# Performance work log

Hardware: AMD Instinct MI355X
Metric: run time of the kernel (lower is better)

Reference implementation:

```python
import jax, jax.numpy as jnp
import numpy as np

N_NODES = 100_000
N_EDGES = 1_600_000
HEADS = 3
DIMS = [6, 8, 16, 32]  # in -> conv1 -> conv2 -> conv3 out_feats


def _edge_gat(x, ef, src, dst, W, We, al, ar, ae, b, n_nodes):
    """DGL EdgeGATConv: edge feats modulate attention logits; messages are alpha * W h_src."""
    H, D = al.shape
    ft = (x @ W.T).reshape(n_nodes, H, D)          # [N,H,D] projected node feats
    fe = (ef @ We.T).reshape(-1, H, D)             # [E,H,D] projected edge feats
    el = jnp.sum(ft * al, axis=-1)                 # [N,H]
    er = jnp.sum(ft * ar, axis=-1)                 # [N,H]
    ee = jnp.sum(fe * ae, axis=-1)                 # [E,H]
    e = jax.nn.leaky_relu(el[src] + er[dst] + ee, 0.2)  # [E,H] (DGL default slope 0.2)
    # segment softmax over incoming edges of each dst node
    m = jax.ops.segment_max(e, dst, num_segments=n_nodes)
    m = jnp.where(jnp.isfinite(m), m, 0.0)         # zero-in-degree nodes
    ex = jnp.exp(e - m[dst])
    denom = jax.ops.segment_sum(ex, dst, num_segments=n_nodes)
    a = ex / jnp.maximum(denom[dst], 1e-9)         # [E,H]
    msg = a[:, :, None] * ft[src]                  # [E,H,D]
    out = jax.ops.segment_sum(msg, dst, num_segments=n_nodes)  # [N,H,D]
    return out + b.reshape(1, H, D)


def setup_inputs() -> dict:
    key = jax.random.key(0)
    ks = jax.random.split(key, 32)
    d = {
        "node_feats": jax.random.normal(ks[0], (N_NODES, DIMS[0]), jnp.float32),
        "edge_feats": jax.random.uniform(ks[1], (N_EDGES, 1), jnp.float32),
        "src": jax.random.randint(ks[2], (N_EDGES,), 0, N_NODES, jnp.int32),
        "dst": jax.random.randint(ks[3], (N_EDGES,), 0, N_NODES, jnp.int32),
    }
    ki = 4
    for i in range(3):
        fin, fout = DIMS[i], DIMS[i + 1]
        s = 1.0 / np.sqrt(fin)
        d[f"W{i+1}"] = jax.random.normal(ks[ki], (HEADS * fout, fin), jnp.float32) * s; ki += 1
        d[f"We{i+1}"] = jax.random.normal(ks[ki], (HEADS * fout, 1), jnp.float32); ki += 1
        d[f"al{i+1}"] = jax.random.normal(ks[ki], (HEADS, fout), jnp.float32) * 0.1; ki += 1
        d[f"ar{i+1}"] = jax.random.normal(ks[ki], (HEADS, fout), jnp.float32) * 0.1; ki += 1
        d[f"ae{i+1}"] = jax.random.normal(ks[ki], (HEADS, fout), jnp.float32) * 0.1; ki += 1
        d[f"b{i+1}"] = jnp.zeros((HEADS * fout,), jnp.float32)
    for name, (fo, fi) in [("l1", (16, 32)), ("l2", (4, 16)), ("l3", (1, 4)), ("l4", (1, HEADS))]:
        s = 1.0 / np.sqrt(fi)
        d[name + "w"] = jax.random.uniform(ks[ki], (fo, fi), jnp.float32, -s, s); ki += 1
        d[name + "b"] = jax.random.uniform(ks[ki], (fo,), jnp.float32, -s, s); ki += 1
    return d


def reference(node_feats, edge_feats, src, dst,
              W1, We1, al1, ar1, ae1, b1,
              W2, We2, al2, ar2, ae2, b2,
              W3, We3, al3, ar3, ae3, b3,
              l1w, l1b, l2w, l2b, l3w, l3b, l4w, l4b):
    n = node_feats.shape[0]
    h1 = _edge_gat(node_feats, edge_feats, src, dst, W1, We1, al1, ar1, ae1, b1, n)  # [N,3,8]
    h2 = _edge_gat(h1.mean(axis=1), edge_feats, src, dst, W2, We2, al2, ar2, ae2, b2, n)  # [N,3,16]
    h3 = _edge_gat(h2.mean(axis=1), edge_feats, src, dst, W3, We3, al3, ar3, ae3, b3, n)  # [N,3,32]
    # per-(node,head) MLP head: 32 -> 16 -> 4 -> 1
    x = jax.nn.leaky_relu(h3 @ l1w.T + l1b, 0.01)
    x = jax.nn.leaky_relu(x @ l2w.T + l2b, 0.01)
    x = x @ l3w.T + l3b                            # [N,3,1]
    feats = x.reshape(n, -1) @ l4w.T + l4b         # [N,1] combine heads
    return jnp.max(feats, axis=0)                  # [1]
```

## Files before the change

### kernel.cpp

```cpp
#include <hip/hip_runtime.h>
#include <hip/hip_bf16.h>
#include <hip/hip_fp16.h>

#define HEADS 3

union HU { uint4 u; __half2 h[4]; };

__global__ void prep_ce_kernel(const float* __restrict__ We1, const float* __restrict__ ae1,
                               const float* __restrict__ We2, const float* __restrict__ ae2,
                               const float* __restrict__ We3, const float* __restrict__ ae3,
                               float* __restrict__ ce) {
    int t = threadIdx.x;
    if (t >= 9) return;
    int l = t / 3, h = t % 3;
    const float* We = (l == 0) ? We1 : (l == 1) ? We2 : We3;
    const float* ae = (l == 0) ? ae1 : (l == 1) ? ae2 : ae3;
    int D = (l == 0) ? 8 : (l == 1) ? 16 : 32;
    float s = 0.f;
    for (int d = 0; d < D; d++) s += We[h * D + d] * ae[h * D + d];
    ce[t] = s;
}

__global__ void hist_rank_kernel(const int* __restrict__ dst, int* __restrict__ deg,
                                 int* __restrict__ rank, int E) {
    int tid = blockIdx.x * blockDim.x + threadIdx.x;
    if (tid < E) rank[tid] = atomicAdd(&deg[dst[tid]], 1);
}

#define SCAN_BLK 1024
__global__ void scan1_kernel(const int* __restrict__ deg, int* __restrict__ row_ptr,
                             int* __restrict__ partials, int N) {
    __shared__ int sm[SCAN_BLK];
    int t = threadIdx.x;
    int g = blockIdx.x * SCAN_BLK + t;
    int v = (g < N) ? deg[g] : 0;
    sm[t] = v;
    __syncthreads();
    for (int off = 1; off < SCAN_BLK; off <<= 1) {
        int x = (t >= off) ? sm[t - off] : 0;
        __syncthreads();
        sm[t] += x;
        __syncthreads();
    }
    if (g < N) row_ptr[g] = sm[t] - v;
    if (t == SCAN_BLK - 1) partials[blockIdx.x] = sm[t];
}

__global__ void scan2_kernel(int* __restrict__ partials, int NB) {
    __shared__ int sm[128];
    int t = threadIdx.x;
    int v = (t < NB) ? partials[t] : 0;
    sm[t] = v;
    __syncthreads();
    for (int off = 1; off < 128; off <<= 1) {
        int x = (t >= off) ? sm[t - off] : 0;
        __syncthreads();
        sm[t] += x;
        __syncthreads();
    }
    if (t < NB) partials[t] = sm[t] - v;
    if (t == 127) partials[NB] = sm[127];
}

__global__ void scan3_kernel(int* __restrict__ row_ptr, const int* __restrict__ partials,
                             int N, int NB) {
    int g = blockIdx.x * SCAN_BLK + threadIdx.x;
    if (g < N) row_ptr[g] += partials[blockIdx.x];
    if (blockIdx.x == 0 && threadIdx.x == 0) row_ptr[N] = partials[NB];
}

__global__ void scatter_kernel(const int* __restrict__ src, const int* __restrict__ dst,
                               const float* __restrict__ ef, const int* __restrict__ row_ptr,
                               const int* __restrict__ rank, int2* __restrict__ erec, int E) {
    int tid = blockIdx.x * blockDim.x + threadIdx.x;
    if (tid >= E) return;
    int d = dst[tid];
    int pos = row_ptr[d] + rank[tid];
    union { int2 r; long long ll; } u;
    u.r.x = src[tid];
    u.r.y = __float_as_int(ef[tid]);
    __builtin_nontemporal_store(u.ll, (long long*)&erec[pos]);
}

template <int FIN, int D>
__launch_bounds__(256)
__global__ void node_kernel(const float* __restrict__ xin,
                            const float* __restrict__ W,
                            const float* __restrict__ al,
                            const float* __restrict__ ar,
                            __half* __restrict__ ft,
                            float* __restrict__ el, float* __restrict__ er,
                            int N) {
    int tid = blockIdx.x * blockDim.x + threadIdx.x;
    if (tid >= N * HEADS) return;
    int n = tid / HEADS, h = tid % HEADS;
    float x[FIN];
    #pragma unroll
    for (int k = 0; k < FIN; k++) x[k] = xin[n * FIN + k];
    float fv[D];
    float e_l = 0.f, e_r = 0.f;
    #pragma unroll
    for (int d = 0; d < D; d++) {
        const float* wr = &W[(h * D + d) * FIN];
        float f = 0.f;
        #pragma unroll
        for (int k = 0; k < FIN; k++) f += x[k] * wr[k];
        fv[d] = f;
        e_l += f * al[h * D + d];
        e_r += f * ar[h * D + d];
    }
    uint4* dst16 = (uint4*)(ft + (size_t)tid * D);
    #pragma unroll
    for (int q = 0; q < D / 8; q++) {
        HU u;
        #pragma unroll
        for (int j = 0; j < 4; j++)
            u.h[j] = __floats2half2_rn(fv[q * 8 + 2 * j], fv[q * 8 + 2 * j + 1]);
        dst16[q] = u.u;
    }
    el[tid] = e_l;
    er[tid] = e_r;
}

template <int D, int EPI>
__launch_bounds__(256)
__global__ void agg_kernel(const int* __restrict__ row_ptr, const int2* __restrict__ erec,
                           const __half* __restrict__ ft,
                           const float* __restrict__ el, const float* __restrict__ er,
                           const float* __restrict__ ce,
                           const float* __restrict__ b,
                           float* __restrict__ xmean,
                           __half* __restrict__ h3out,
                           int N) {
    int w = threadIdx.x >> 6;
    int l = threadIdx.x & 63;
    int wl = l / 6;
    int rem = l - wl * 6;
    int s = rem >= 3 ? 1 : 0;
    int h = rem - s * 3;
    int n = (blockIdx.x * 4 + w) * 10 + wl;
    bool active = (wl < 10) && (n < N);

    float m = -3.0e38f, ssum = 0.f;
    float msg[D];
    #pragma unroll
    for (int d = 0; d < D; d++) msg[d] = 0.f;
    int unit = n * HEADS + h;
    float ceh = ce[h];

    if (active) {
        int beg = row_ptr[n], end = row_ptr[n + 1];
        int cnt = end - beg;
        int half = (cnt + 1) >> 1;
        int es = beg + s * half;
        int ee = s ? end : (beg + half);
        float ern = er[unit];

        int e = es;
        for (; e + 3 < ee; e += 4) {
            int2 r0 = erec[e + 0], r1 = erec[e + 1], r2 = erec[e + 2], r3 = erec[e + 3];
            float v0 = el[r0.x * HEADS + h] + ern + __int_as_float(r0.y) * ceh;
            float v1 = el[r1.x * HEADS + h] + ern + __int_as_float(r1.y) * ceh;
            float v2 = el[r2.x * HEADS + h] + ern + __int_as_float(r2.y) * ceh;
            float v3 = el[r3.x * HEADS + h] + ern + __int_as_float(r3.y) * ceh;
            v0 = v0 > 0.f ? v0 : 0.2f * v0;
            v1 = v1 > 0.f ? v1 : 0.2f * v1;
            v2 = v2 > 0.f ? v2 : 0.2f * v2;
            v3 = v3 > 0.f ? v3 : 0.2f * v3;
            float cm = fmaxf(fmaxf(v0, v1), fmaxf(v2, v3));
            if (cm > m) {
                float sc = __expf(m - cm);
                ssum *= sc;
                #pragma unroll
                for (int d = 0; d < D; d++) msg[d] *= sc;
                m = cm;
            }
            float x0 = __expf(v0 - m), x1 = __expf(v1 - m);
            float x2 = __expf(v2 - m), x3 = __expf(v3 - m);
            ssum += (x0 + x1) + (x2 + x3);
            const uint4* f0 = (const uint4*)(ft + ((size_t)r0.x * HEADS + h) * D);
            const uint4* f1 = (const uint4*)(ft + ((size_t)r1.x * HEADS + h) * D);
            const uint4* f2 = (const uint4*)(ft + ((size_t)r2.x * HEADS + h) * D);
            const uint4* f3 = (const uint4*)(ft + ((size_t)r3.x * HEADS + h) * D);
            #pragma unroll
            for (int q = 0; q < D / 8; q++) {
                HU a0, a1, a2, a3;
                a0.u = f0[q]; a1.u = f1[q]; a2.u = f2[q]; a3.u = f3[q];
                #pragma unroll
                for (int j = 0; j < 4; j++) {
                    float2 p0 = __half22float2(a0.h[j]);
                    float2 p1 = __half22float2(a1.h[j]);
                    float2 p2 = __half22float2(a2.h[j]);
                    float2 p3 = __half22float2(a3.h[j]);
                    msg[q * 8 + 2 * j + 0] += x0 * p0.x + x1 * p1.x + x2 * p2.x + x3 * p3.x;
                    msg[q * 8 + 2 * j + 1] += x0 * p0.y + x1 * p1.y + x2 * p2.y + x3 * p3.y;
                }
            }
        }
        for (; e < ee; e++) {
            int2 r = erec[e];
            float v = el[r.x * HEADS + h] + ern + __int_as_float(r.y) * ceh;
            v = v > 0.f ? v : 0.2f * v;
            if (v > m) {
                float sc = __expf(m - v);
                ssum *= sc;
                #pragma unroll
                for (int d = 0; d < D; d++) msg[d] *= sc;
                m = v;
            }
            float x = __expf(v - m);
            ssum += x;
            const uint4* fr = (const uint4*)(ft + ((size_t)r.x * HEADS + h) * D);
            #pragma unroll
            for (int q = 0; q < D / 8; q++) {
                HU a; a.u = fr[q];
                #pragma unroll
                for (int j = 0; j < 4; j++) {
                    float2 p = __half22float2(a.h[j]);
                    msg[q * 8 + 2 * j + 0] += x * p.x;
                    msg[q * 8 + 2 * j + 1] += x * p.y;
                }
            }
        }
    }

    int pl = (s ? (l - 3) : (l + 3)) & 63;
    float om = __shfl(m, pl);
    float osum = __shfl(ssum, pl);
    float M = fmaxf(m, om);
    float sA = __expf(m - M);
    float sB = __expf(om - M);
    float tot = ssum * sA + osum * sB;
    float inv = 1.0f / fmaxf(tot, 1e-9f);
    #pragma unroll
    for (int d = 0; d < D; d++)
        msg[d] = (msg[d] * sA + __shfl(msg[d], pl) * sB) * inv + b[h * D + d];

    if (EPI == 0) {
        int g0 = wl * 6 + s * 3;
        #pragma unroll
        for (int d = 0; d < D; d++)
            msg[d] = (__shfl(msg[d], g0) + __shfl(msg[d], g0 + 1) + __shfl(msg[d], g0 + 2)) * (1.0f / 3.0f);
        if (active && h == 0) {
            int lo = s * (D / 2);
            float* ob = xmean + (size_t)n * D + lo;
            #pragma unroll
            for (int d = 0; d < D / 2; d += 4) {
                float4 v;
                v.x = msg[lo + d + 0]; v.y = msg[lo + d + 1];
                v.z = msg[lo + d + 2]; v.w = msg[lo + d + 3];
                *(float4*)(ob + d) = v;
            }
        }
    } else {
        if (active) {
            int lo = s * (D / 2);
            __half* hb = h3out + ((size_t)n * HEADS + h) * D + lo;
            #pragma unroll
            for (int q = 0; q < D / 16; q++) {
                HU u;
                #pragma unroll
                for (int j = 0; j < 4; j++)
                    u.h[j] = __floats2half2_rn(msg[lo + q * 8 + 2 * j],
                                               msg[lo + q * 8 + 2 * j + 1]);
                *(uint4*)(hb + q * 8) = u.u;
            }
        }
    }
}

__global__ void mlp_max_kernel(const __half* __restrict__ h3,
                               const float* __restrict__ l1w, const float* __restrict__ l1b,
                               const float* __restrict__ l2w, const float* __restrict__ l2b,
                               const float* __restrict__ l3w, const float* __restrict__ l3b,
                               const float* __restrict__ l4w, const float* __restrict__ l4b,
                               unsigned int* __restrict__ maxkey, int N) {
    int tid = blockIdx.x * blockDim.x + threadIdx.x;
    float feat = -3.0e38f;
    if (tid < N) {
        float acc = l4b[0];
        #pragma unroll
        for (int h = 0; h < HEADS; h++) {
            const uint4* vp = (const uint4*)(h3 + ((size_t)tid * HEADS + h) * 32);
            float v[32];
            #pragma unroll
            for (int q = 0; q < 4; q++) {
                HU a; a.u = vp[q];
                #pragma unroll
                for (int j = 0; j < 4; j++) {
                    float2 p = __half22float2(a.h[j]);
                    v[q * 8 + 2 * j + 0] = p.x;
                    v[q * 8 + 2 * j + 1] = p.y;
                }
            }
            float y1[16];
            #pragma unroll
            for (int i = 0; i < 16; i++) {
                float s = l1b[i];
                const float* w = &l1w[i * 32];
                #pragma unroll
                for (int k = 0; k < 32; k++) s += v[k] * w[k];
                y1[i] = s > 0.f ? s : 0.01f * s;
            }
            float y2[4];
            #pragma unroll
            for (int i = 0; i < 4; i++) {
                float s = l2b[i];
                const float* w = &l2w[i * 16];
                #pragma unroll
                for (int k = 0; k < 16; k++) s += y1[k] * w[k];
                y2[i] = s > 0.f ? s : 0.01f * s;
            }
            float y3 = l3b[0];
            #pragma unroll
            for (int k = 0; k < 4; k++) y3 += y2[k] * l3w[k];
            acc += y3 * l4w[h];
        }
        feat = acc;
    }
    #pragma unroll
    for (int off = 32; off > 0; off >>= 1)
        feat = fmaxf(feat, __shfl_down(feat, off));
    if ((threadIdx.x & 63) == 0) {
        unsigned int u = __float_as_uint(feat);
        unsigned int key = (u & 0x80000000u) ? ~u : (u | 0x80000000u);
        atomicMax(maxkey, key);
    }
}

__global__ void finalize_kernel(const unsigned int* __restrict__ maxkey, float* __restrict__ out) {
    unsigned int key = *maxkey;
    unsigned int u = (key & 0x80000000u) ? (key & 0x7FFFFFFFu) : ~key;
    out[0] = __uint_as_float(u);
}

extern "C" void kernel_launch(void* const* d_in, const int* in_sizes, int n_in,
                              void* d_out, int out_size, void* d_ws, size_t ws_size,
                              hipStream_t stream) {
    const float* node_feats = (const float*)d_in[0];
    const float* edge_feats = (const float*)d_in[1];
    const int* src = (const int*)d_in[2];
    const int* dst = (const int*)d_in[3];
    const float* W1  = (const float*)d_in[4];
    const float* We1 = (const float*)d_in[5];
    const float* al1 = (const float*)d_in[6];
    const float* ar1 = (const float*)d_in[7];
    const float* ae1 = (const float*)d_in[8];
    const float* b1  = (const float*)d_in[9];
    const float* W2  = (const float*)d_in[10];
    const float* We2 = (const float*)d_in[11];
    const float* al2 = (const float*)d_in[12];
    const float* ar2 = (const float*)d_in[13];
    const float* ae2 = (const float*)d_in[14];
    const float* b2  = (const float*)d_in[15];
    const float* W3  = (const float*)d_in[16];
    const float* We3 = (const float*)d_in[17];
    const float* al3 = (const float*)d_in[18];
    const float* ar3 = (const float*)d_in[19];
    const float* ae3 = (const float*)d_in[20];
    const float* b3  = (const float*)d_in[21];
    const float* l1w = (const float*)d_in[22];
    const float* l1b = (const float*)d_in[23];
    const float* l2w = (const float*)d_in[24];
    const float* l2b = (const float*)d_in[25];
    const float* l3w = (const float*)d_in[26];
    const float* l3b = (const float*)d_in[27];
    const float* l4w = (const float*)d_in[28];
    const float* l4b = (const float*)d_in[29];

    const int N = in_sizes[0] / 6;
    const int E = in_sizes[2];
    const int NB = (N + SCAN_BLK - 1) / SCAN_BLK;

    char* ws = (char*)d_ws;
    size_t off = 0;
    auto alloc = [&](size_t bytes) -> void* {
        void* p = ws + off;
        off = (off + bytes + 255) & ~(size_t)255;
        return p;
    };
    int* deg            = (int*)alloc((size_t)N * 4);
    unsigned int* mkey  = (unsigned int*)alloc(4);
    size_t zero_bytes   = off;
    int* rank           = (int*)alloc((size_t)E * 4);
    int* row_ptr        = (int*)alloc((size_t)(N + 1) * 4);
    int* partials       = (int*)alloc((size_t)(NB + 1) * 4);
    int2* erec          = (int2*)alloc((size_t)E * 8);
    __half* ft          = (__half*)alloc((size_t)N * 96 * 2);
    __half* h3          = (__half*)alloc((size_t)N * 96 * 2);
    float* xmean        = (float*)alloc((size_t)N * 16 * 4);
    float* el           = (float*)alloc((size_t)N * 3 * 4);
    float* er           = (float*)alloc((size_t)N * 3 * 4);
    float* ce           = (float*)alloc(9 * 4);

    hipMemsetAsync(d_ws, 0, zero_bytes, stream);

    prep_ce_kernel<<<1, 16, 0, stream>>>(We1, ae1, We2, ae2, We3, ae3, ce);
    hist_rank_kernel<<<(E + 255) / 256, 256, 0, stream>>>(dst, deg, rank, E);
    scan1_kernel<<<NB, SCAN_BLK, 0, stream>>>(deg, row_ptr, partials, N);
    scan2_kernel<<<1, 128, 0, stream>>>(partials, NB);
    scan3_kernel<<<NB, SCAN_BLK, 0, stream>>>(row_ptr, partials, N, NB);
    scatter_kernel<<<(E + 255) / 256, 256, 0, stream>>>(src, dst, edge_feats, row_ptr, rank,
                                                        erec, E);

    const int NH = N * HEADS;
    const int gb = (NH + 255) / 256;
    const int gb_agg = (N + 39) / 40;

    node_kernel<6, 8><<<gb, 256, 0, stream>>>(node_feats, W1, al1, ar1, ft, el, er, N);
    agg_kernel<8, 0><<<gb_agg, 256, 0, stream>>>(row_ptr, erec, ft, el, er, ce + 0, b1,
                                                 xmean, nullptr, N);
    node_kernel<8, 16><<<gb, 256, 0, stream>>>(xmean, W2, al2, ar2, ft, el, er, N);
    agg_kernel<16, 0><<<gb_agg, 256, 0, stream>>>(row_ptr, erec, ft, el, er, ce + 3, b2,
                                                  xmean, nullptr, N);
    node_kernel<16, 32><<<gb, 256, 0, stream>>>(xmean, W3, al3, ar3, ft, el, er, N);
    agg_kernel<32, 1><<<gb_agg, 256, 0, stream>>>(row_ptr, erec, ft, el, er, ce + 6, b3,
                                                  nullptr, h3, N);

    mlp_max_kernel<<<(N + 255) / 256, 256, 0, stream>>>(h3, l1w, l1b, l2w, l2b, l3w, l3b,
                                                        l4w, l4b, mkey, N);
    finalize_kernel<<<1, 1, 0, stream>>>(mkey, (float*)d_out);
}
```

Baseline: 463.7 us.

## Sort aggregation nodes by degree and pack layer-1 features with logits

Adds a counting sort of nodes by in-degree (histogram, scan, scatter) so each wavefront in the aggregation kernels processes nodes of similar degree, which reduces lane divergence from imbalanced edge loops. For layer 1, the projected half-precision features and the el logits are packed into one 64-byte record per node, so each gathered source node costs one cache line instead of separate ft and el accesses. This adds three small preprocessing kernels and makes aggregation output writes scattered rather than contiguous.

```diff
diff --git a/kernel.cpp b/kernel.cpp
--- a/kernel.cpp
+++ b/kernel.cpp
@@ -82,12 +82,66 @@
     __builtin_nontemporal_store(u.ll, (long long*)&erec[pos]);
 }
 
-template <int FIN, int D>
+#define OCHUNK 1024
+__global__ void obhist_kernel(const int* __restrict__ deg, int* __restrict__ bh,
+                              int N, int nblk) {
+    __shared__ int hist[64];
+    int t = threadIdx.x;
+    if (t < 64) hist[t] = 0;
+    __syncthreads();
+    int base = blockIdx.x * OCHUNK;
+    for (int i = t; i < OCHUNK; i += 256) {
+        int g = base + i;
+        if (g < N) atomicAdd(&hist[min(deg[g], 63)], 1);
+    }
+    __syncthreads();
+    if (t < 64) bh[t * nblk + blockIdx.x] = hist[t];
+}
+
+__global__ void oscan_kernel(int* __restrict__ bh, int M) {
+    __shared__ int sums[256];
+    int t = threadIdx.x;
+    int C = (M + 255) / 256;
+    int b = t * C, e = min(b + C, M);
+    int s = 0;
+    for (int i = b; i < e; i++) s += bh[i];
+    sums[t] = s;
+    __syncthreads();
+    for (int off = 1; off < 256; off <<= 1) {
+        int x = (t >= off) ? sums[t - off] : 0;
+        __syncthreads();
+        sums[t] += x;
+        __syncthreads();
+    }
+    int run = sums[t] - s;
+    for (int i = b; i < e; i++) { int v = bh[i]; bh[i] = run; run += v; }
+}
+
+__global__ void oscatter_kernel(const int* __restrict__ deg, const int* __restrict__ bh,
+                                int* __restrict__ order, int N, int nblk) {
+    __shared__ int base_[64];
+    __shared__ int cnt_[64];
+    int t = threadIdx.x;
+    if (t < 64) { base_[t] = bh[t * nblk + blockIdx.x]; cnt_[t] = 0; }
+    __syncthreads();
+    int cbase = blockIdx.x * OCHUNK;
+    for (int i = t; i < OCHUNK; i += 256) {
+        int g = cbase + i;
+        if (g < N) {
+            int bin = min(deg[g], 63);
+            int off = atomicAdd(&cnt_[bin], 1);
+            order[base_[bin] + off] = g;
+        }
+    }
+}
+
+template <int FIN, int D, int RECB>
 __launch_bounds__(256)
 __global__ void node_kernel(const float* __restrict__ xin,
                             const float* __restrict__ W,
                             const float* __restrict__ al,
                             const float* __restrict__ ar,
+                            char* __restrict__ rec,
                             __half* __restrict__ ft,
                             float* __restrict__ el, float* __restrict__ er,
                             int N) {
@@ -109,22 +163,38 @@
         e_l += f * al[h * D + d];
         e_r += f * ar[h * D + d];
     }
-    uint4* dst16 = (uint4*)(ft + (size_t)tid * D);
-    #pragma unroll
-    for (int q = 0; q < D / 8; q++) {
-        HU u;
+    if (RECB > 0) {
+        char* rp = rec + (size_t)n * RECB;
+        uint4* dst16 = (uint4*)(rp + h * (D * 2));
         #pragma unroll
-        for (int j = 0; j < 4; j++)
-            u.h[j] = __floats2half2_rn(fv[q * 8 + 2 * j], fv[q * 8 + 2 * j + 1]);
-        dst16[q] = u.u;
-    }
-    el[tid] = e_l;
+        for (int q = 0; q < D / 8; q++) {
+            HU u;
+            #pragma unroll
+            for (int j = 0; j < 4; j++)
+                u.h[j] = __floats2half2_rn(fv[q * 8 + 2 * j], fv[q * 8 + 2 * j + 1]);
+            dst16[q] = u.u;
+        }
+        *(float*)(rp + 3 * D * 2 + h * 4) = e_l;
+    } else {
+        uint4* dst16 = (uint4*)(ft + (size_t)tid * D);
+        #pragma unroll
+        for (int q = 0; q < D / 8; q++) {
+            HU u;
+            #pragma unroll
+            for (int j = 0; j < 4; j++)
+                u.h[j] = __floats2half2_rn(fv[q * 8 + 2 * j], fv[q * 8 + 2 * j + 1]);
+            dst16[q] = u.u;
+        }
+        el[tid] = e_l;
+    }
     er[tid] = e_r;
 }
 
-template <int D, int EPI>
+template <int D, int RECB, int EPI>
 __launch_bounds__(256)
 __global__ void agg_kernel(const int* __restrict__ row_ptr, const int2* __restrict__ erec,
+                           const int* __restrict__ order,
+                           const char* __restrict__ rec,
                            const __half* __restrict__ ft,
                            const float* __restrict__ el, const float* __restrict__ er,
                            const float* __restrict__ ce,
@@ -132,14 +202,16 @@
                            float* __restrict__ xmean,
                            __half* __restrict__ h3out,
                            int N) {
+    const int ELOFF = 3 * D * 2;
     int w = threadIdx.x >> 6;
     int l = threadIdx.x & 63;
     int wl = l / 6;
     int rem = l - wl * 6;
     int s = rem >= 3 ? 1 : 0;
     int h = rem - s * 3;
-    int n = (blockIdx.x * 4 + w) * 10 + wl;
-    bool active = (wl < 10) && (n < N);
+    int slot = (blockIdx.x * 4 + w) * 10 + wl;
+    bool active = (wl < 10) && (slot < N);
+    int n = active ? order[slot] : 0;
 
     float m = -3.0e38f, ssum = 0.f;
     float msg[D];
@@ -159,10 +231,25 @@
         int e = es;
         for (; e + 3 < ee; e += 4) {
             int2 r0 = erec[e + 0], r1 = erec[e + 1], r2 = erec[e + 2], r3 = erec[e + 3];
-            float v0 = el[r0.x * HEADS + h] + ern + __int_as_float(r0.y) * ceh;
-            float v1 = el[r1.x * HEADS + h] + ern + __int_as_float(r1.y) * ceh;
-            float v2 = el[r2.x * HEADS + h] + ern + __int_as_float(r2.y) * ceh;
-            float v3 = el[r3.x * HEADS + h] + ern + __int_as_float(r3.y) * ceh;
+            const char* p0; const char* p1; const char* p2; const char* p3;
+            float v0, v1, v2, v3;
+            if (RECB > 0) {
+                p0 = rec + (size_t)r0.x * RECB; p1 = rec + (size_t)r1.x * RECB;
+                p2 = rec + (size_t)r2.x * RECB; p3 = rec + (size_t)r3.x * RECB;
+                v0 = *(const float*)(p0 + ELOFF + h * 4) + ern + __int_as_float(r0.y) * ceh;
+                v1 = *(const float*)(p1 + ELOFF + h * 4) + ern + __int_as_float(r1.y) * ceh;
+                v2 = *(const float*)(p2 + ELOFF + h * 4) + ern + __int_as_float(r2.y) * ceh;
+                v3 = *(const float*)(p3 + ELOFF + h * 4) + ern + __int_as_float(r3.y) * ceh;
+            } else {
+                p0 = (const char*)(ft + ((size_t)r0.x * HEADS + h) * D);
+                p1 = (const char*)(ft + ((size_t)r1.x * HEADS + h) * D);
+                p2 = (const char*)(ft + ((size_t)r2.x * HEADS + h) * D);
+                p3 = (const char*)(ft + ((size_t)r3.x * HEADS + h) * D);
+                v0 = el[r0.x * HEADS + h] + ern + __int_as_float(r0.y) * ceh;
+                v1 = el[r1.x * HEADS + h] + ern + __int_as_float(r1.y) * ceh;
+                v2 = el[r2.x * HEADS + h] + ern + __int_as_float(r2.y) * ceh;
+                v3 = el[r3.x * HEADS + h] + ern + __int_as_float(r3.y) * ceh;
+            }
             v0 = v0 > 0.f ? v0 : 0.2f * v0;
             v1 = v1 > 0.f ? v1 : 0.2f * v1;
             v2 = v2 > 0.f ? v2 : 0.2f * v2;
@@ -178,28 +265,36 @@
             float x0 = __expf(v0 - m), x1 = __expf(v1 - m);
             float x2 = __expf(v2 - m), x3 = __expf(v3 - m);
             ssum += (x0 + x1) + (x2 + x3);
-            const uint4* f0 = (const uint4*)(ft + ((size_t)r0.x * HEADS + h) * D);
-            const uint4* f1 = (const uint4*)(ft + ((size_t)r1.x * HEADS + h) * D);
-            const uint4* f2 = (const uint4*)(ft + ((size_t)r2.x * HEADS + h) * D);
-            const uint4* f3 = (const uint4*)(ft + ((size_t)r3.x * HEADS + h) * D);
+            const uint4* f0 = (const uint4*)(RECB > 0 ? p0 + h * (D * 2) : p0);
+            const uint4* f1 = (const uint4*)(RECB > 0 ? p1 + h * (D * 2) : p1);
+            const uint4* f2 = (const uint4*)(RECB > 0 ? p2 + h * (D * 2) : p2);
+            const uint4* f3 = (const uint4*)(RECB > 0 ? p3 + h * (D * 2) : p3);
             #pragma unroll
             for (int q = 0; q < D / 8; q++) {
                 HU a0, a1, a2, a3;
                 a0.u = f0[q]; a1.u = f1[q]; a2.u = f2[q]; a3.u = f3[q];
                 #pragma unroll
                 for (int j = 0; j < 4; j++) {
-                    float2 p0 = __half22float2(a0.h[j]);
-                    float2 p1 = __half22float2(a1.h[j]);
-                    float2 p2 = __half22float2(a2.h[j]);
-                    float2 p3 = __half22float2(a3.h[j]);
-                    msg[q * 8 + 2 * j + 0] += x0 * p0.x + x1 * p1.x + x2 * p2.x + x3 * p3.x;
-                    msg[q * 8 + 2 * j + 1] += x0 * p0.y + x1 * p1.y + x2 * p2.y + x3 * p3.y;
+                    float2 p0v = __half22float2(a0.h[j]);
+                    float2 p1v = __half22float2(a1.h[j]);
+                    float2 p2v = __half22float2(a2.h[j]);
+                    float2 p3v = __half22float2(a3.h[j]);
+                    msg[q * 8 + 2 * j + 0] += x0 * p0v.x + x1 * p1v.x + x2 * p2v.x + x3 * p3v.x;
+                    msg[q * 8 + 2 * j + 1] += x0 * p0v.y + x1 * p1v.y + x2 * p2v.y + x3 * p3v.y;
                 }
             }
         }
         for (; e < ee; e++) {
             int2 r = erec[e];
-            float v = el[r.x * HEADS + h] + ern + __int_as_float(r.y) * ceh;
+            const char* pr;
+            float v;
+            if (RECB > 0) {
+                pr = rec + (size_t)r.x * RECB;
+                v = *(const float*)(pr + ELOFF + h * 4) + ern + __int_as_float(r.y) * ceh;
+            } else {
+                pr = (const char*)(ft + ((size_t)r.x * HEADS + h) * D);
+                v = el[r.x * HEADS + h] + ern + __int_as_float(r.y) * ceh;
+            }
             v = v > 0.f ? v : 0.2f * v;
             if (v > m) {
                 float sc = __expf(m - v);
@@ -210,7 +305,7 @@
             }
             float x = __expf(v - m);
             ssum += x;
-            const uint4* fr = (const uint4*)(ft + ((size_t)r.x * HEADS + h) * D);
+            const uint4* fr = (const uint4*)(RECB > 0 ? pr + h * (D * 2) : pr);
             #pragma unroll
             for (int q = 0; q < D / 8; q++) {
                 HU a; a.u = fr[q];
@@ -371,6 +466,7 @@
     const int N = in_sizes[0] / 6;
     const int E = in_sizes[2];
     const int NB = (N + SCAN_BLK - 1) / SCAN_BLK;
+    const int NOB = (N + OCHUNK - 1) / OCHUNK;
 
     char* ws = (char*)d_ws;
     size_t off = 0;
@@ -385,7 +481,10 @@
     int* rank           = (int*)alloc((size_t)E * 4);
     int* row_ptr        = (int*)alloc((size_t)(N + 1) * 4);
     int* partials       = (int*)alloc((size_t)(NB + 1) * 4);
+    int* bh             = (int*)alloc((size_t)(64 * NOB + 1) * 4);
+    int* order          = (int*)alloc((size_t)N * 4);
     int2* erec          = (int2*)alloc((size_t)E * 8);
+    char* rec1          = (char*)alloc((size_t)N * 64);
     __half* ft          = (__half*)alloc((size_t)N * 96 * 2);
     __half* h3          = (__half*)alloc((size_t)N * 96 * 2);
     float* xmean        = (float*)alloc((size_t)N * 16 * 4);
@@ -402,20 +501,24 @@
     scan3_kernel<<<NB, SCAN_BLK, 0, stream>>>(row_ptr, partials, N, NB);
     scatter_kernel<<<(E + 255) / 256, 256, 0, stream>>>(src, dst, edge_feats, row_ptr, rank,
                                                         erec, E);
+    obhist_kernel<<<NOB, 256, 0, stream>>>(deg, bh, N, NOB);
+    oscan_kernel<<<1, 256, 0, stream>>>(bh, 64 * NOB);
+    oscatter_kernel<<<NOB, 256, 0, stream>>>(deg, bh, order, N, NOB);
 
     const int NH = N * HEADS;
     const int gb = (NH + 255) / 256;
     const int gb_agg = (N + 39) / 40;
 
-    node_kernel<6, 8><<<gb, 256, 0, stream>>>(node_feats, W1, al1, ar1, ft, el, er, N);
-    agg_kernel<8, 0><<<gb_agg, 256, 0, stream>>>(row_ptr, erec, ft, el, er, ce + 0, b1,
-                                                 xmean, nullptr, N);
-    node_kernel<8, 16><<<gb, 256, 0, stream>>>(xmean, W2, al2, ar2, ft, el, er, N);
-    agg_kernel<16, 0><<<gb_agg, 256, 0, stream>>>(row_ptr, erec, ft, el, er, ce + 3, b2,
-                                                  xmean, nullptr, N);
-    node_kernel<16, 32><<<gb, 256, 0, stream>>>(xmean, W3, al3, ar3, ft, el, er, N);
-    agg_kernel<32, 1><<<gb_agg, 256, 0, stream>>>(row_ptr, erec, ft, el, er, ce + 6, b3,
-                                                  nullptr, h3, N);
+    node_kernel<6, 8, 64><<<gb, 256, 0, stream>>>(node_feats, W1, al1, ar1, rec1, nullptr,
+                                                  nullptr, er, N);
+    agg_kernel<8, 64, 0><<<gb_agg, 256, 0, stream>>>(row_ptr, erec, order, rec1, nullptr,
+                                                     nullptr, er, ce + 0, b1, xmean, nullptr, N);
+    node_kernel<8, 16, 0><<<gb, 256, 0, stream>>>(xmean, W2, al2, ar2, nullptr, ft, el, er, N);
+    agg_kernel<16, 0, 0><<<gb_agg, 256, 0, stream>>>(row_ptr, erec, order, nullptr, ft,
+                                                     el, er, ce + 3, b2, xmean, nullptr, N);
+    node_kernel<16, 32, 0><<<gb, 256, 0, stream>>>(xmean, W3, al3, ar3, nullptr, ft, el, er, N);
+    agg_kernel<32, 0, 1><<<gb_agg, 256, 0, stream>>>(row_ptr, erec, order, nullptr, ft,
+                                                     el, er, ce + 6, b3, nullptr, h3, N);
 
     mlp_max_kernel<<<(N + 255) / 256, 256, 0, stream>>>(h3, l1w, l1b, l2w, l2b, l3w, l3b,
                                                         l4w, l4b, mkey, N);
```

Result: slower. 476.7 us (+2.8%).
